# Optimization experiments

Measured on AMD Instinct MI355X. Metric: run time of the kernel, lower is better.

Reference implementation:

```python
import jax, jax.numpy as jnp
import numpy as np

R_RAYS = 65536
S_PER_RAY = 128
N_TOTAL = R_RAYS * S_PER_RAY


def setup_inputs() -> dict:
    key = jax.random.key(0)
    k1, k2, k3, k4 = jax.random.split(key, 4)
    sigmas = jax.random.uniform(k1, (N_TOTAL,), dtype=jnp.float32) * 2.0  # densities >= 0
    rgbs = jax.random.uniform(k2, (N_TOTAL, 3), dtype=jnp.float32)
    deltas = jax.random.uniform(k3, (N_TOTAL,), dtype=jnp.float32) * 0.01 + 1e-3
    ts = jax.random.uniform(k4, (N_TOTAL,), dtype=jnp.float32) * 6.0 + 0.1
    ray_idx = jnp.arange(R_RAYS, dtype=jnp.int32)
    rays_a = jnp.stack([ray_idx, ray_idx * S_PER_RAY,
                        jnp.full((R_RAYS,), S_PER_RAY, dtype=jnp.int32)], axis=1)
    return {"sigmas": sigmas, "rgbs": rgbs, "deltas": deltas, "ts": ts,
            "rays_a": rays_a, "T_threshold": 1e-4}


def reference(sigmas, rgbs, deltas, ts, rays_a, T_threshold):
    R = rays_a.shape[0]
    N = sigmas.shape[0]
    S_max = int(jnp.max(rays_a[:, 2]))  # max samples per ray (concrete)

    offs = jnp.arange(S_max, dtype=rays_a.dtype)
    valid = offs[None, :] < rays_a[:, 2, None]              # [R, S] prefix mask
    idx = jnp.where(valid, rays_a[:, 1, None] + offs[None, :], N - 1)  # [R, S]

    a = 1.0 - jnp.exp(-sigmas[idx] * deltas[idx])           # [R, S] alphas

    # Sequential transmittance recurrence with early-exit (T set to 0 once below threshold)
    def step(T, xs):
        a_s, v_s = xs                                        # [R], [R]
        alive = (T > T_threshold) & v_s
        w = jnp.where(alive, a_s * T, 0.0)
        T = jnp.where(alive, T * (1.0 - a_s), 0.0)
        return T, (w, alive)

    T0 = jnp.ones((R,), sigmas.dtype)
    _, (wT, aliveT) = jax.lax.scan(step, T0, (a.T, valid.T))
    w = wT.T                                                 # [R, S] weights
    alive = aliveT.T

    op_n = jnp.sum(w, axis=1)                                # [R]
    dep_n = jnp.sum(w * ts[idx], axis=1)                     # [R]
    rgb_n = jnp.einsum('rs,rsc->rc', w, rgbs[idx])           # [R, 3]
    cnt_n = jnp.sum(alive, axis=1).astype(jnp.int32)

    ridx = rays_a[:, 0]
    opacity = jnp.zeros((R,), w.dtype).at[ridx].add(op_n)
    depth = jnp.zeros((R,), w.dtype).at[ridx].add(dep_n)
    rgb = jnp.zeros((R, 3), w.dtype).at[ridx].add(rgb_n)
    total_samples = jnp.zeros((R,), jnp.int32).at[ridx].add(cnt_n)
    # invalid slots were mapped to index N-1 with w=0, so .add is safe
    ws = jnp.zeros((N,), w.dtype).at[idx.reshape(-1)].add(w.reshape(-1))

    return total_samples.sum(), opacity, depth, rgb, ws
```

## Files before the change

### kernel.cpp

```cpp
#include <hip/hip_runtime.h>


#define NIT 4

typedef float f4a __attribute__((ext_vector_type(4), aligned(4)));

template<int CTRL, int RM, unsigned OLD>
__device__ __forceinline__ float dpp_f(float v) {
    return __int_as_float(__builtin_amdgcn_update_dpp(
        (int)OLD, __float_as_int(v), CTRL, RM, 0xF, false));
}

__device__ __forceinline__ float seg_sum32_hi(float v) {
    v += dpp_f<0x111, 0xF, 0u>(v);
    v += dpp_f<0x112, 0xF, 0u>(v);
    v += dpp_f<0x114, 0xF, 0u>(v);
    v += dpp_f<0x118, 0xF, 0u>(v);
    v += dpp_f<0x142, 0xA, 0u>(v);
    return v;
}

struct Ld { float4 sg, dt, tt, c0, c1, c2; };

__device__ __forceinline__ Ld load_ray(
    const float* __restrict__ sigmas, const float* __restrict__ deltas,
    const float* __restrict__ ts, const float* __restrict__ rgbs,
    int start, int count, bool inR, int sl, bool fastw)
{
    Ld d;
    if (fastw) {
        d.sg = *(const float4*)(sigmas + start + 4 * sl);
        d.dt = *(const float4*)(deltas + start + 4 * sl);
        d.tt = *(const float4*)(ts     + start + 4 * sl);
        const float* rg = rgbs + 3 * ((size_t)start + 4 * sl);
        d.c0 = *(const float4*)(rg + 0);
        d.c1 = *(const float4*)(rg + 4);
        d.c2 = *(const float4*)(rg + 8);
    } else {
        float sg[4], dt[4], tt[4], rr[4], gg[4], bb[4];
        #pragma unroll
        for (int i = 0; i < 4; ++i) {
            const int s = 4 * sl + i;
            const bool vi = inR && (s < count);
            sg[i] = dt[i] = tt[i] = rr[i] = gg[i] = bb[i] = 0.f;
            if (vi) {
                sg[i] = sigmas[start + s];
                dt[i] = deltas[start + s];
                tt[i] = ts[start + s];
                const float* rg = rgbs + 3 * ((size_t)start + s);
                rr[i] = rg[0]; gg[i] = rg[1]; bb[i] = rg[2];
            }
        }
        d.sg = make_float4(sg[0], sg[1], sg[2], sg[3]);
        d.dt = make_float4(dt[0], dt[1], dt[2], dt[3]);
        d.tt = make_float4(tt[0], tt[1], tt[2], tt[3]);
        d.c0 = make_float4(rr[0], gg[0], bb[0], rr[1]);
        d.c1 = make_float4(gg[1], bb[1], rr[2], gg[2]);
        d.c2 = make_float4(bb[2], rr[3], gg[3], bb[3]);
    }
    return d;
}

__device__ __forceinline__ void compute_ray(
    const Ld& d, int ridx, int start, int count, int ray, bool inR, bool fastw,
    int sl, float thr, float* __restrict__ out, float* __restrict__ cnt_ws,
    int R, int use_ws)
{
    float fe[4] = { __expf(-d.sg.x * d.dt.x), __expf(-d.sg.y * d.dt.y),
                    __expf(-d.sg.z * d.dt.z), __expf(-d.sg.w * d.dt.w) };
    bool v[4];
    #pragma unroll
    for (int i = 0; i < 4; ++i) v[i] = inR && (4 * sl + i) < count;

    const float fprod = (fe[0] * fe[1]) * (fe[2] * fe[3]);
    float inc = fprod;
    inc *= dpp_f<0x111, 0xF, 0x3f800000u>(inc);
    inc *= dpp_f<0x112, 0xF, 0x3f800000u>(inc);
    inc *= dpp_f<0x114, 0xF, 0x3f800000u>(inc);
    inc *= dpp_f<0x118, 0xF, 0x3f800000u>(inc);
    inc *= dpp_f<0x142, 0xA, 0x3f800000u>(inc);

    float ex = dpp_f<0x138, 0xF, 0x3f800000u>(inc);
    float T = (sl == 0) ? 1.f : ex;

    float w[4];
    float cnt = 0.f;
    #pragma unroll
    for (int i = 0; i < 4; ++i) {
        const bool alive = v[i] && (T > thr);
        const float Tn = T * fe[i];
        w[i] = alive ? (T - Tn) : 0.f;
        cnt += alive ? 1.f : 0.f;
        T = Tn;
    }

    float* wsp = out + 1 + 5 * (size_t)R + (size_t)start + 4 * sl;
    if (fastw) {
        f4a wv; wv.x = w[0]; wv.y = w[1]; wv.z = w[2]; wv.w = w[3];
        *(f4a*)wsp = wv;
    } else {
        #pragma unroll
        for (int i = 0; i < 4; ++i) if (v[i]) wsp[i] = w[i];
    }

    float op  = (w[0] + w[1]) + (w[2] + w[3]);
    float dep = fmaf(w[0], d.tt.x, fmaf(w[1], d.tt.y, fmaf(w[2], d.tt.z, w[3] * d.tt.w)));
    float cr  = fmaf(w[0], d.c0.x, fmaf(w[1], d.c0.w, fmaf(w[2], d.c1.z, w[3] * d.c2.y)));
    float cg  = fmaf(w[0], d.c0.y, fmaf(w[1], d.c1.x, fmaf(w[2], d.c1.w, w[3] * d.c2.z)));
    float cb  = fmaf(w[0], d.c0.z, fmaf(w[1], d.c1.y, fmaf(w[2], d.c2.x, w[3] * d.c2.w)));

    op  = seg_sum32_hi(op);
    dep = seg_sum32_hi(dep);
    cr  = seg_sum32_hi(cr);
    cg  = seg_sum32_hi(cg);
    cb  = seg_sum32_hi(cb);
    cnt = seg_sum32_hi(cnt);

    if (sl == 31 && inR) {
        out[1 + ridx]                 = op;
        out[1 + R + ridx]             = dep;
        out[1 + 2 * R + 3 * ridx + 0] = cr;
        out[1 + 2 * R + 3 * ridx + 1] = cg;
        out[1 + 2 * R + 3 * ridx + 2] = cb;
        if (use_ws) cnt_ws[ray] = cnt;
        else        atomicAdd(&out[0], cnt);
    }
}

__global__ __launch_bounds__(256) void vr_main(
    const float* __restrict__ sigmas, const float* __restrict__ rgbs,
    const float* __restrict__ deltas, const float* __restrict__ ts,
    const int* __restrict__ rays_a, const float* __restrict__ thr_p,
    float* __restrict__ out, float* __restrict__ cnt_ws,
    int R, int use_ws)
{
    const int wib  = (int)(threadIdx.x >> 6);
    const int lane = (int)(threadIdx.x & 63);
    const int half = lane >> 5;
    const int sl   = lane & 31;
    const int wid  = (int)blockIdx.x * 4 + wib;
    const int wpg  = (int)gridDim.x * 4;
    const float thr = thr_p[0];

    int ridx[NIT], start[NIT], count[NIT], rayk[NIT];
    bool inR[NIT], fw[NIT];
    #pragma unroll
    for (int k = 0; k < NIT; ++k) {
        const int ray = 2 * (wid + k * wpg) + half;
        rayk[k] = ray;
        inR[k] = ray < R;
        ridx[k] = start[k] = count[k] = 0;
        if (inR[k]) {
            ridx[k]  = rays_a[3 * ray + 0];
            start[k] = rays_a[3 * ray + 1];
            count[k] = rays_a[3 * ray + 2];
        }
    }
    #pragma unroll
    for (int k = 0; k < NIT; ++k)
        fw[k] = __all(inR[k] && (count[k] == 128) && ((start[k] & 3) == 0));

    Ld A = load_ray(sigmas, deltas, ts, rgbs, start[0], count[0], inR[0], sl, fw[0]);
    #pragma unroll
    for (int k = 0; k < NIT; ++k) {
        if (k + 1 < NIT) {
            Ld B = load_ray(sigmas, deltas, ts, rgbs,
                            start[k + 1], count[k + 1], inR[k + 1], sl, fw[k + 1]);
            compute_ray(A, ridx[k], start[k], count[k], rayk[k], inR[k], fw[k],
                        sl, thr, out, cnt_ws, R, use_ws);
            A = B;
        } else {
            compute_ray(A, ridx[k], start[k], count[k], rayk[k], inR[k], fw[k],
                        sl, thr, out, cnt_ws, R, use_ws);
        }
    }
}

__global__ __launch_bounds__(1024) void vr_total(
    const float* __restrict__ cnt_ws, float* __restrict__ out, int R)
{
    __shared__ float sm[16];
    float s = 0.f;
    const int R4 = R & ~3;
    for (int i = (int)threadIdx.x * 4; i < R4; i += 4096) {
        const float4 c = *(const float4*)(cnt_ws + i);
        s += (c.x + c.y) + (c.z + c.w);
    }
    if (threadIdx.x == 0)
        for (int i = R4; i < R; ++i) s += cnt_ws[i];
    #pragma unroll
    for (int d = 32; d; d >>= 1) s += __shfl_xor(s, d, 64);
    if ((threadIdx.x & 63) == 0) sm[threadIdx.x >> 6] = s;
    __syncthreads();
    if (threadIdx.x == 0) {
        float t = 0.f;
        #pragma unroll
        for (int k = 0; k < 16; ++k) t += sm[k];
        out[0] = t;
    }
}

extern "C" void kernel_launch(void* const* d_in, const int* in_sizes, int n_in,
                              void* d_out, int out_size, void* d_ws, size_t ws_size,
                              hipStream_t stream) {
    const float* sigmas = (const float*)d_in[0];
    const float* rgbs   = (const float*)d_in[1];
    const float* deltas = (const float*)d_in[2];
    const float* ts     = (const float*)d_in[3];
    const int*   rays_a = (const int*)d_in[4];
    const float* thr    = (const float*)d_in[5];
    int R = in_sizes[4] / 3;
    float* out = (float*)d_out;
    float* cnt_ws = (float*)d_ws;

    int use_ws = (ws_size >= (size_t)R * sizeof(float)) ? 1 : 0;

    if (!use_ws)
        hipMemsetAsync(d_out, 0, 4, stream);

    const int raysPerBlock = 8 * NIT;
    int grid = (R + raysPerBlock - 1) / raysPerBlock;
    vr_main<<<grid, 256, 0, stream>>>(sigmas, rgbs, deltas, ts, rays_a, thr,
                                      out, cnt_ws, R, use_ws);
    if (use_ws)
        vr_total<<<1, 1024, 0, stream>>>(cnt_ws, out, R);
}
```

Measured before the change: 47.73 us.

## Speculatively prefetch ray samples at the assumed ray*128 offset before reading rays_a

Each wave now handles a single ray pair and issues its vector loads at a guessed start offset (ray*128) before the rays_a metadata arrives. It then checks the guess against the real start and count and falls back to the general scalar-load path when they differ, so the dependent-load latency at kernel start is hidden. The multi-ray software pipeline per wave is dropped, giving a larger grid. Per-ray sample counts are now reduced inside each block through shared memory, so the final reduction kernel only sums one value per block. The speculation wastes bandwidth and adds a second load when rays are not laid out contiguously.

```diff
diff --git a/kernel.cpp b/kernel.cpp
--- a/kernel.cpp
+++ b/kernel.cpp
@@ -1,7 +1,7 @@
 #include <hip/hip_runtime.h>
 
 
-#define NIT 4
+#define BW 4
 
 typedef float f4a __attribute__((ext_vector_type(4), aligned(4)));
 
@@ -22,21 +22,46 @@
 
 struct Ld { float4 sg, dt, tt, c0, c1, c2; };
 
-__device__ __forceinline__ Ld load_ray(
-    const float* __restrict__ sigmas, const float* __restrict__ deltas,
-    const float* __restrict__ ts, const float* __restrict__ rgbs,
-    int start, int count, bool inR, int sl, bool fastw)
+__global__ __launch_bounds__(256) void vr_main(
+    const float* __restrict__ sigmas, const float* __restrict__ rgbs,
+    const float* __restrict__ deltas, const float* __restrict__ ts,
+    const int* __restrict__ rays_a, const float* __restrict__ thr_p,
+    float* __restrict__ out, float* __restrict__ blk_ws,
+    int R, int use_ws, int spec_ok)
 {
+    __shared__ float bsum[BW];
+
+    const int wib  = (int)(threadIdx.x >> 6);
+    const int wid  = (int)blockIdx.x * BW + wib;
+    const int lane = (int)(threadIdx.x & 63);
+    const int half = lane >> 5;
+    const int sl   = lane & 31;
+    const int ray  = 2 * wid + half;
+    const bool inR = ray < R;
+    const float thr = thr_p[0];
+
+    const int p_start = ray << 7;
     Ld d;
-    if (fastw) {
-        d.sg = *(const float4*)(sigmas + start + 4 * sl);
-        d.dt = *(const float4*)(deltas + start + 4 * sl);
-        d.tt = *(const float4*)(ts     + start + 4 * sl);
-        const float* rg = rgbs + 3 * ((size_t)start + 4 * sl);
+    if (spec_ok && inR) {
+        d.sg = *(const float4*)(sigmas + p_start + 4 * sl);
+        d.dt = *(const float4*)(deltas + p_start + 4 * sl);
+        d.tt = *(const float4*)(ts     + p_start + 4 * sl);
+        const float* rg = rgbs + 3 * ((size_t)p_start + 4 * sl);
         d.c0 = *(const float4*)(rg + 0);
         d.c1 = *(const float4*)(rg + 4);
         d.c2 = *(const float4*)(rg + 8);
-    } else {
+    }
+
+    int ridx = 0, start = 0, count = 0;
+    if (inR) {
+        ridx  = rays_a[3 * ray + 0];
+        start = rays_a[3 * ray + 1];
+        count = rays_a[3 * ray + 2];
+    }
+    const bool match = spec_ok && inR && (start == p_start) && (count == 128);
+    const bool fastw = __all(match);
+
+    if (!fastw) {
         float sg[4], dt[4], tt[4], rr[4], gg[4], bb[4];
         #pragma unroll
         for (int i = 0; i < 4; ++i) {
@@ -58,14 +83,7 @@
         d.c1 = make_float4(gg[1], bb[1], rr[2], gg[2]);
         d.c2 = make_float4(bb[2], rr[3], gg[3], bb[3]);
     }
-    return d;
-}
 
-__device__ __forceinline__ void compute_ray(
-    const Ld& d, int ridx, int start, int count, int ray, bool inR, bool fastw,
-    int sl, float thr, float* __restrict__ out, float* __restrict__ cnt_ws,
-    int R, int use_ws)
-{
     float fe[4] = { __expf(-d.sg.x * d.dt.x), __expf(-d.sg.y * d.dt.y),
                     __expf(-d.sg.z * d.dt.z), __expf(-d.sg.w * d.dt.w) };
     bool v[4];
@@ -122,82 +140,31 @@
         out[1 + 2 * R + 3 * ridx + 0] = cr;
         out[1 + 2 * R + 3 * ridx + 1] = cg;
         out[1 + 2 * R + 3 * ridx + 2] = cb;
-        if (use_ws) cnt_ws[ray] = cnt;
-        else        atomicAdd(&out[0], cnt);
+    }
+
+    const float cw =
+        __int_as_float(__builtin_amdgcn_readlane(__float_as_int(cnt), 31)) +
+        __int_as_float(__builtin_amdgcn_readlane(__float_as_int(cnt), 63));
+    if (lane == 0) bsum[wib] = cw;
+    __syncthreads();
+    if (threadIdx.x == 0) {
+        const float t = (bsum[0] + bsum[1]) + (bsum[2] + bsum[3]);
+        if (use_ws) blk_ws[blockIdx.x] = t;
+        else        atomicAdd(&out[0], t);
     }
 }
 
-__global__ __launch_bounds__(256) void vr_main(
-    const float* __restrict__ sigmas, const float* __restrict__ rgbs,
-    const float* __restrict__ deltas, const float* __restrict__ ts,
-    const int* __restrict__ rays_a, const float* __restrict__ thr_p,
-    float* __restrict__ out, float* __restrict__ cnt_ws,
-    int R, int use_ws)
+__global__ __launch_bounds__(256) void vr_total(
+    const float* __restrict__ blk_ws, float* __restrict__ out, int nb)
 {
-    const int wib  = (int)(threadIdx.x >> 6);
-    const int lane = (int)(threadIdx.x & 63);
-    const int half = lane >> 5;
-    const int sl   = lane & 31;
-    const int wid  = (int)blockIdx.x * 4 + wib;
-    const int wpg  = (int)gridDim.x * 4;
-    const float thr = thr_p[0];
-
-    int ridx[NIT], start[NIT], count[NIT], rayk[NIT];
-    bool inR[NIT], fw[NIT];
-    #pragma unroll
-    for (int k = 0; k < NIT; ++k) {
-        const int ray = 2 * (wid + k * wpg) + half;
-        rayk[k] = ray;
-        inR[k] = ray < R;
-        ridx[k] = start[k] = count[k] = 0;
-        if (inR[k]) {
-            ridx[k]  = rays_a[3 * ray + 0];
-            start[k] = rays_a[3 * ray + 1];
-            count[k] = rays_a[3 * ray + 2];
-        }
-    }
-    #pragma unroll
-    for (int k = 0; k < NIT; ++k)
-        fw[k] = __all(inR[k] && (count[k] == 128) && ((start[k] & 3) == 0));
-
-    Ld A = load_ray(sigmas, deltas, ts, rgbs, start[0], count[0], inR[0], sl, fw[0]);
-    #pragma unroll
-    for (int k = 0; k < NIT; ++k) {
-        if (k + 1 < NIT) {
-            Ld B = load_ray(sigmas, deltas, ts, rgbs,
-                            start[k + 1], count[k + 1], inR[k + 1], sl, fw[k + 1]);
-            compute_ray(A, ridx[k], start[k], count[k], rayk[k], inR[k], fw[k],
-                        sl, thr, out, cnt_ws, R, use_ws);
-            A = B;
-        } else {
-            compute_ray(A, ridx[k], start[k], count[k], rayk[k], inR[k], fw[k],
-                        sl, thr, out, cnt_ws, R, use_ws);
-        }
-    }
-}
-
-__global__ __launch_bounds__(1024) void vr_total(
-    const float* __restrict__ cnt_ws, float* __restrict__ out, int R)
-{
-    __shared__ float sm[16];
+    __shared__ float sm[4];
     float s = 0.f;
-    const int R4 = R & ~3;
-    for (int i = (int)threadIdx.x * 4; i < R4; i += 4096) {
-        const float4 c = *(const float4*)(cnt_ws + i);
-        s += (c.x + c.y) + (c.z + c.w);
-    }
-    if (threadIdx.x == 0)
-        for (int i = R4; i < R; ++i) s += cnt_ws[i];
+    for (int i = (int)threadIdx.x; i < nb; i += 256) s += blk_ws[i];
     #pragma unroll
     for (int d = 32; d; d >>= 1) s += __shfl_xor(s, d, 64);
     if ((threadIdx.x & 63) == 0) sm[threadIdx.x >> 6] = s;
     __syncthreads();
-    if (threadIdx.x == 0) {
-        float t = 0.f;
-        #pragma unroll
-        for (int k = 0; k < 16; ++k) t += sm[k];
-        out[0] = t;
-    }
+    if (threadIdx.x == 0) out[0] = (sm[0] + sm[1]) + (sm[2] + sm[3]);
 }
 
 extern "C" void kernel_launch(void* const* d_in, const int* in_sizes, int n_in,
@@ -209,19 +176,23 @@
     const float* ts     = (const float*)d_in[3];
     const int*   rays_a = (const int*)d_in[4];
     const float* thr    = (const float*)d_in[5];
-    int R = in_sizes[4] / 3;
+    const int R = in_sizes[4] / 3;
     float* out = (float*)d_out;
-    float* cnt_ws = (float*)d_ws;
+    float* blk_ws = (float*)d_ws;
 
-    int use_ws = (ws_size >= (size_t)R * sizeof(float)) ? 1 : 0;
+    const int grid = (R + 2 * BW - 1) / (2 * BW);
+    const int use_ws = (ws_size >= (size_t)grid * sizeof(float)) ? 1 : 0;
+
+    const long long need = (long long)R * 128;
+    const int spec_ok = (in_sizes[0] >= need) && (in_sizes[2] >= need) &&
+                        (in_sizes[3] >= need) &&
+                        ((long long)in_sizes[1] >= 3 * need);
 
     if (!use_ws)
         hipMemsetAsync(d_out, 0, 4, stream);
 
-    const int raysPerBlock = 8 * NIT;
-    int grid = (R + raysPerBlock - 1) / raysPerBlock;
     vr_main<<<grid, 256, 0, stream>>>(sigmas, rgbs, deltas, ts, rays_a, thr,
-                                      out, cnt_ws, R, use_ws);
+                                      out, blk_ws, R, use_ws, spec_ok);
     if (use_ws)
-        vr_total<<<1, 1024, 0, stream>>>(cnt_ws, out, R);
+        vr_total<<<1, 256, 0, stream>>>(blk_ws, out, grid);
 }
```

Result: slower. 49.12 us (+2.9%).
